# Performance work log

Measured on AMD Instinct MI355X. Metric: run time of the kernel, lower is better.

Reference implementation:

```python
import jax, jax.numpy as jnp
import numpy as np

B, O, T = 32, 256, 1024
D_OBJ = 512      # obj_input_dim
D_PRED = 512     # predicate_input_dim
HID = 512        # hidden_dim
P_OUT = 512      # predicate_output_dim
OBJ_OUT = 512    # object_output_dim
N_PRED_TYPES = 50
ORIGINAL_EDGE = 0
TRANSITIVE_EDGE = 1


def setup_inputs() -> dict:
    key = jax.random.key(0)
    ks = jax.random.split(key, 16)

    def kaiming(k, fan_in, fan_out):
        return jax.random.normal(k, (fan_in, fan_out), jnp.float32) * np.sqrt(2.0 / fan_in)

    n1_in = 2 * D_OBJ + D_PRED            # 1536
    n1_out = 2 * HID + P_OUT              # 1536
    return {
        "obj_vecs": jax.random.normal(ks[0], (B, O, D_OBJ), jnp.float32),
        "pred_vecs": jax.random.normal(ks[1], (B, T, D_PRED), jnp.float32),
        "W1a": kaiming(ks[2], n1_in, HID), "b1a": jnp.zeros((HID,), jnp.float32),
        "W1b": kaiming(ks[3], HID, n1_out), "b1b": jnp.zeros((n1_out,), jnp.float32),
        "W2a": kaiming(ks[4], HID, HID), "b2a": jnp.zeros((HID,), jnp.float32),
        "W2b": kaiming(ks[5], HID, OBJ_OUT), "b2b": jnp.zeros((OBJ_OUT,), jnp.float32),
        "pt_weights": jax.random.normal(ks[6], (N_PRED_TYPES,), jnp.float32),
        "edges": jax.random.randint(ks[7], (B, T, 2), 0, O, jnp.int32),
        "pred_indicators": jax.random.randint(ks[8], (B, T), 0, 2, jnp.int32).astype(bool),
        "triplet_type": jax.random.randint(ks[9], (B, T), 0, 2, jnp.int32),
        "predicate_ids": jax.random.randint(ks[10], (B, T), 0, N_PRED_TYPES, jnp.int32),
    }


def reference(obj_vecs, pred_vecs, W1a, b1a, W1b, b1b, W2a, b2a, W2b, b2b,
              pt_weights, edges, pred_indicators, triplet_type, predicate_ids):
    s_idx = edges[:, :, 0]  # [B,T]
    o_idx = edges[:, :, 1]

    # gather subject/object vectors: [B,T,D]
    cur_s = jnp.take_along_axis(obj_vecs, s_idx[:, :, None], axis=1)
    cur_o = jnp.take_along_axis(obj_vecs, o_idx[:, :, None], axis=1)
    cur_t = jnp.concatenate([cur_s, pred_vecs, cur_o], axis=-1)  # [B,T,2D+Dp]

    # net1: Linear-ReLU-Linear-ReLU
    h = jax.nn.relu(cur_t @ W1a + b1a)
    new_t = jax.nn.relu(h @ W1b + b1b)  # [B,T,2*HID+P_OUT]

    # confidence weighting
    pt_pred = jax.nn.sigmoid(pt_weights)  # [N_PRED_TYPES]
    conf = ((triplet_type == ORIGINAL_EDGE).astype(jnp.float32)
            + (triplet_type == TRANSITIVE_EDGE).astype(jnp.float32) * pt_pred[predicate_ids])  # [B,T]
    new_t = new_t * conf[:, :, None]

    new_s = new_t[:, :, :HID]
    new_p = new_t[:, :, HID:HID + P_OUT]
    new_o = new_t[:, :, HID + P_OUT:]

    mask = pred_indicators.astype(jnp.float32)  # [B,T]

    def pool_one(si, oi, sv, ov, cf, m):
        # masked scatter-add (equivalent to torch boolean-masked scatter_add)
        sums = (jax.ops.segment_sum(sv * m[:, None], si, num_segments=O)
                + jax.ops.segment_sum(ov * m[:, None], oi, num_segments=O))  # [O,HID]
        w = cf * m
        counts = (jax.ops.segment_sum(w, si, num_segments=O)
                  + jax.ops.segment_sum(w, oi, num_segments=O))  # [O]
        nz = counts > 0
        return jnp.where(nz[:, None], sums / jnp.where(nz, counts, 1.0)[:, None], sums)

    pooled = jax.vmap(pool_one)(s_idx, o_idx, new_s, new_o, conf, mask)  # [B,O,HID]

    # net2: Linear-ReLU-Linear-ReLU
    h2 = jax.nn.relu(pooled @ W2a + b2a)
    new_obj = jax.nn.relu(h2 @ W2b + b2b)  # [B,O,OBJ_OUT]

    return new_obj, new_p
```

## Files before the change

kernel.cpp:

```cpp
#include <hip/hip_runtime.h>
#include <hip/hip_bf16.h>
#include <cstdint>
#include <cstddef>

#define DEV __device__ __forceinline__

typedef __attribute__((ext_vector_type(8))) short  s8v;
typedef __attribute__((ext_vector_type(4))) float  f4v;
typedef __attribute__((ext_vector_type(4))) uint32_t u4v;

DEV unsigned short f2bf(float x) {
  union { float f; uint32_t u; } v; v.f = x;
  uint32_t u = v.u + 0x7FFFu + ((v.u >> 16) & 1u);
  return (unsigned short)(u >> 16);
}
DEV uint32_t cvtpk2(float lo, float hi) {
  uint32_t r;
  asm("v_cvt_pk_bf16_f32 %0, %1, %2" : "=v"(r) : "v"(lo), "v"(hi));
  return r;
}
DEV unsigned short f2bf_fast(float x) { return (unsigned short)cvtpk2(x, 0.f); }
DEV float bf2f(unsigned short b) {
  union { uint32_t u; float f; } v; v.u = ((uint32_t)b) << 16;
  return v.f;
}

DEV void async_copy16(void* lds, const void* g) {
  typedef __attribute__((address_space(3))) uint32_t lds_t;
  typedef const __attribute__((address_space(1))) uint32_t g_t;
  __builtin_amdgcn_global_load_lds((g_t*)g, (lds_t*)lds, 16, 0, 0);
}

#define WAITV4()    asm volatile("s_waitcnt vmcnt(4)" ::: "memory")
#define WAITV0()    asm volatile("s_waitcnt vmcnt(0)" ::: "memory")
#define MEMFENCE()  asm volatile("" ::: "memory")

constexpr int Bc = 32, Oc = 256, Tc = 1024;
constexpr int BM = 128, BN = 128, BK = 64;
constexpr int CSR_CAP = 46;

DEV void swz_mn(int nyb, int* mb, int* nb) {
  const int nwg = gridDim.x * gridDim.y;
  const int w   = blockIdx.x + blockIdx.y * gridDim.x;
  const int cpx = nwg >> 3;
  const int s   = (w & 7) * cpx + (w >> 3);
  *mb = s / nyb;
  *nb = s % nyb;
}

__global__ __launch_bounds__(256)
void cvt_k(const float* __restrict__ in, unsigned short* __restrict__ outp, int n8)
{
  const int i = blockIdx.x * 256 + threadIdx.x;
  if (i >= n8) return;
  const f4v v0 = *(const f4v*)(in + (size_t)i * 8);
  const f4v v1 = *(const f4v*)(in + (size_t)i * 8 + 4);
  u4v pk;
  pk.x = cvtpk2(v0.x, v0.y);
  pk.y = cvtpk2(v0.z, v0.w);
  pk.z = cvtpk2(v1.x, v1.y);
  pk.w = cvtpk2(v1.z, v1.w);
  *(u4v*)(outp + (size_t)i * 8) = pk;
}

#define READ_A(QM, DST) do {                                                    \
    _Pragma("unroll")                                                           \
    for (int i = 0; i < 4; ++i) {                                               \
      const int row = wm * 128 + ((QM) * 4 + i) * 16 + (lane & 15);             \
      _Pragma("unroll")                                                         \
      for (int kk = 0; kk < 2; ++kk) {                                          \
        const int c = kk * 4 + (lane >> 4);                                     \
        DST[i][kk] = *(const s8v*)(Ab_ + row * 128 + ((c ^ (row & 7)) << 4));   \
      }                                                                         \
    }                                                                           \
  } while (0)

#define READ_B(QN, DST) do {                                                    \
    _Pragma("unroll")                                                           \
    for (int j = 0; j < 2; ++j) {                                               \
      const int row = wn * 64 + ((QN) * 2 + j) * 16 + (lane & 15);              \
      _Pragma("unroll")                                                         \
      for (int kk = 0; kk < 2; ++kk) {                                          \
        const int c = kk * 4 + (lane >> 4);                                     \
        DST[j][kk] = *(const s8v*)(Bb_ + row * 128 + ((c ^ (row & 7)) << 4));   \
      }                                                                         \
    }                                                                           \
  } while (0)

#define SYNC_MFMA(QM, QN, AF, BF) do {                                          \
    MEMFENCE();                                                                 \
    __builtin_amdgcn_s_barrier();                                               \
    asm volatile("s_waitcnt lgkmcnt(0)" ::: "memory");                          \
    __builtin_amdgcn_sched_barrier(0);                                          \
    __builtin_amdgcn_s_setprio(1);                                              \
    _Pragma("unroll")                                                           \
    for (int i = 0; i < 4; ++i)                                                 \
      _Pragma("unroll")                                                         \
      for (int j = 0; j < 2; ++j)                                               \
        _Pragma("unroll")                                                       \
        for (int kk = 0; kk < 2; ++kk)                                          \
          acc[(QM) * 4 + i][(QN) * 2 + j] =                                     \
            __builtin_amdgcn_mfma_f32_16x16x32_bf16(                            \
              AF[i][kk], BF[j][kk], acc[(QM) * 4 + i][(QN) * 2 + j], 0, 0, 0);  \
    __builtin_amdgcn_s_setprio(0);                                              \
  } while (0)

#define ENDPHASE() do { MEMFENCE(); __builtin_amdgcn_s_barrier(); } while (0)

#define KTILE_BODY() do {                                                       \
    const int par = t & 1, px = par ^ 1;                                        \
    const char* Ab_ = smem + par * 65536;                                       \
    const char* Bb_ = Ab_ + 32768;                                              \
    const bool s1 = (t + 1 < nk), s2 = (t + 2 < nk);                            \
                                                                        \
    READ_A(0, af); READ_B(0, bf0);                                              \
    if (s1) stageA(px, 1, t + 1);                                               \
    SYNC_MFMA(0, 0, af, bf0);                                                   \
    ENDPHASE();                                                                 \
                                                                        \
    READ_B(1, bf1);                                                             \
    if (s1) stageB(px, 1, t + 1);                                               \
    SYNC_MFMA(0, 1, af, bf1);                                                   \
    ENDPHASE();                                                                 \
                                                                        \
    READ_A(1, af);                                                              \
    if (s2) stageA(par, 0, t + 2);                                              \
    SYNC_MFMA(1, 1, af, bf1);                                                   \
    ENDPHASE();                                                                 \
                                                                        \
    if (s2) stageB(par, 0, t + 2);                                              \
    SYNC_MFMA(1, 0, af, bf0);                                                   \
    if (s2) { WAITV4(); } else if (s1) { WAITV0(); }                            \
    ENDPHASE();                                                                 \
  } while (0)

template<int EPI>
__global__ __launch_bounds__(512, 2)
void gemm8_k(const unsigned short* __restrict__ Abf,
             const unsigned short* __restrict__ Bt,
             const float* __restrict__ bias,
             const float* __restrict__ conf,
             unsigned short* __restrict__ out_bf,
             float* __restrict__ out_f32,
             unsigned short* __restrict__ out_bf2,
             int M, int N, int K)
{
  __shared__ __align__(16) char smem[131072];

  const int tid = threadIdx.x, lane = tid & 63, wave = tid >> 6;
  const int wm = wave >> 2, wn = wave & 3;
  int mb, nb; swz_mn(gridDim.y, &mb, &nb);
  const int m0 = mb * 256, n0 = nb * 256;
  const int rl  = tid >> 3;
  const int cs8 = ((lane & 7) ^ (lane >> 3)) * 8;
  const int rB0 = (rl >> 5) * 64 + (rl & 31);

  const unsigned short* srcA = Abf + (size_t)(m0 + rl) * K + cs8;
  const unsigned short* srcB = Bt  + (size_t)(n0 + rB0) * K + cs8;

  auto stageA = [&](int p, int qm, int kt) {
    const int k0 = kt * 64;
    #pragma unroll
    for (int s = 0; s < 2; ++s)
      async_copy16(smem + p * 65536 + ((s * 128 + qm * 64 + wave * 8) << 7),
                   srcA + (size_t)(s * 128 + qm * 64) * K + k0);
  };
  auto stageB = [&](int p, int qn, int kt) {
    const int k0 = kt * 64;
    #pragma unroll
    for (int s = 0; s < 2; ++s)
      async_copy16(smem + p * 65536 + 32768 +
                     ((s * 128 + qn * 32 + (wave >> 2) * 64 + (wave & 3) * 8) << 7),
                   srcB + (size_t)(s * 128 + qn * 32) * K + k0);
  };

  f4v acc[8][4] = {};
  s8v af[4][2], bf0[2][2], bf1[2][2];
  const int nk = K / 64;

  stageA(0, 0, 0); stageB(0, 0, 0); stageA(0, 1, 0); stageB(0, 1, 0);
  stageA(1, 0, 1); stageB(1, 0, 1);
  WAITV4();
  MEMFENCE();
  __builtin_amdgcn_s_barrier();

  for (int t = 0; t < nk; ++t) KTILE_BODY();

  const int cn = lane & 15, rq4 = (lane >> 4) * 4;
  #pragma unroll
  for (int f = 0; f < 8; ++f) {
    const int gr0 = m0 + wm * 128 + f * 16 + rq4;
    #pragma unroll
    for (int g = 0; g < 4; ++g) {
      const int gc = n0 + wn * 64 + g * 16 + cn;
      const float bv = bias[gc];
      #pragma unroll
      for (int r = 0; r < 4; ++r) {
        float val = acc[f][g][r] + bv;
        val = val > 0.f ? val : 0.f;
        const int gr = gr0 + r;
        if (EPI == 1) {
          val *= conf[gr];
          if (gc < 512)        out_bf [(size_t)gr * 512 + gc]          = f2bf_fast(val);
          else if (gc < 1024)  out_f32[(size_t)gr * 512 + (gc - 512)]  = val;
          else                 out_bf2[(size_t)gr * 512 + (gc - 1024)] = f2bf_fast(val);
        } else {
          out_bf[(size_t)gr * N + gc] = f2bf_fast(val);
        }
      }
    }
  }
}

__global__ __launch_bounds__(512, 2)
void gemm8g_k(const unsigned short* __restrict__ objb,
              const unsigned short* __restrict__ predb,
              const int* __restrict__ edges,
              const unsigned short* __restrict__ Bt,
              const float* __restrict__ bias,
              unsigned short* __restrict__ outp)
{
  __shared__ __align__(16) char smem[131072];

  const int tid = threadIdx.x, lane = tid & 63, wave = tid >> 6;
  const int wm = wave >> 2, wn = wave & 3;
  int mb, nb; swz_mn(gridDim.y, &mb, &nb);
  const int m0 = mb * 256, n0 = nb * 256;
  const int rl  = tid >> 3;
  const int cs8 = ((lane & 7) ^ (lane >> 3)) * 8;
  const int rB0 = (rl >> 5) * 64 + (rl & 31);

  uint32_t offS[4], offP[4], offO[4];
  #pragma unroll
  for (int c2 = 0; c2 < 4; ++c2) {
    const int r = (c2 >> 1) * 128 + (c2 & 1) * 64 + rl;
    const int m = m0 + r;
    const int ob = (m >> 10) * Oc;
    offS[c2] = (uint32_t)((ob + edges[2 * m])     * 1024 + cs8 * 2);
    offO[c2] = (uint32_t)((ob + edges[2 * m + 1]) * 1024 + cs8 * 2);
    offP[c2] = (uint32_t)(m * 1024 + cs8 * 2);
  }
  const unsigned short* srcB = Bt + (size_t)(n0 + rB0) * 1536 + cs8;

  auto stageA = [&](int p, int qm, int kt) {
    const int reg = kt >> 3;
    const uint32_t koff = (uint32_t)(kt & 7) * 128u;
    #pragma unroll
    for (int s = 0; s < 2; ++s) {
      const int c2 = s * 2 + qm;
      const char* src;
      if (reg == 0)      src = (const char*)objb  + offS[c2] + koff;
      else if (reg == 1) src = (const char*)predb + offP[c2] + koff;
      else               src = (const char*)objb  + offO[c2] + koff;
      async_copy16(smem + p * 65536 + ((s * 128 + qm * 64 + wave * 8) << 7), src);
    }
  };
  auto stageB = [&](int p, int qn, int kt) {
    #pragma unroll
    for (int s = 0; s < 2; ++s)
      async_copy16(smem + p * 65536 + 32768 +
                     ((s * 128 + qn * 32 + (wave >> 2) * 64 + (wave & 3) * 8) << 7),
                   srcB + (size_t)(s * 128 + qn * 32) * 1536 + kt * 64);
  };

  f4v acc[8][4] = {};
  s8v af[4][2], bf0[2][2], bf1[2][2];
  constexpr int nk = 24;

  stageA(0, 0, 0); stageB(0, 0, 0); stageA(0, 1, 0); stageB(0, 1, 0);
  stageA(1, 0, 1); stageB(1, 0, 1);
  WAITV4();
  MEMFENCE();
  __builtin_amdgcn_s_barrier();

  for (int t = 0; t < nk; ++t) KTILE_BODY();

  const int cn = lane & 15, rq4 = (lane >> 4) * 4;
  #pragma unroll
  for (int f = 0; f < 8; ++f) {
    const int gr0 = m0 + wm * 128 + f * 16 + rq4;
    #pragma unroll
    for (int g = 0; g < 4; ++g) {
      const int gc = n0 + wn * 64 + g * 16 + cn;
      const float bv = bias[gc];
      #pragma unroll
      for (int r = 0; r < 4; ++r) {
        float val = acc[f][g][r] + bv;
        val = val > 0.f ? val : 0.f;
        outp[(size_t)(gr0 + r) * 512 + gc] = f2bf_fast(val);
      }
    }
  }
}

template<int EPI>
__global__ __launch_bounds__(256)
void gemm_k(const unsigned short* __restrict__ Abf,
            const unsigned short* __restrict__ Bt,
            const float* __restrict__ bias,
            unsigned short* __restrict__ out_bf,
            float* __restrict__ out_f32,
            int M, int N, int K)
{
  __shared__ __align__(16) char smem[BM * BK * 2 + BN * BK * 2];
  char* As = smem;
  char* Bs = smem + BM * BK * 2;

  const int tid  = threadIdx.x;
  const int lane = tid & 63;
  const int wave = tid >> 6;
  const int wm = wave >> 1, wn = wave & 1;
  int mb, nb; swz_mn(gridDim.y, &mb, &nb);
  const int m0 = mb * BM;
  const int n0 = nb * BN;

  f4v acc[4][4] = {};

  for (int k0 = 0; k0 < K; k0 += BK) {
    {
      const int r8 = lane >> 3;
      const int cs = (lane & 7) ^ r8;
      const unsigned short* src = Bt + (size_t)(n0 + wave * 32 + r8) * K + k0 + cs * 8;
      #pragma unroll
      for (int i = 0; i < 4; ++i)
        async_copy16(Bs + (wave * 32 + i * 8) * 128, src + (size_t)i * 8 * K);
      const unsigned short* srca = Abf + (size_t)(m0 + wave * 32 + r8) * K + k0 + cs * 8;
      #pragma unroll
      for (int i = 0; i < 4; ++i)
        async_copy16(As + (wave * 32 + i * 8) * 128, srca + (size_t)i * 8 * K);
    }
    __syncthreads();

    #pragma unroll
    for (int kk = 0; kk < 2; ++kk) {
      s8v af[4], bfv[4];
      #pragma unroll
      for (int i = 0; i < 4; ++i) {
        const int row = wm * 64 + i * 16 + (lane & 15);
        const int c = kk * 4 + (lane >> 4);
        af[i] = *(const s8v*)(As + row * 128 + ((c ^ (row & 7)) << 4));
      }
      #pragma unroll
      for (int j = 0; j < 4; ++j) {
        const int row = wn * 64 + j * 16 + (lane & 15);
        const int c = kk * 4 + (lane >> 4);
        bfv[j] = *(const s8v*)(Bs + row * 128 + ((c ^ (row & 7)) << 4));
      }
      #pragma unroll
      for (int i = 0; i < 4; ++i)
        #pragma unroll
        for (int j = 0; j < 4; ++j)
          acc[i][j] = __builtin_amdgcn_mfma_f32_16x16x32_bf16(af[i], bfv[j], acc[i][j], 0, 0, 0);
    }
    __syncthreads();
  }

  const int cn = lane & 15, rq4 = (lane >> 4) * 4;
  #pragma unroll
  for (int i = 0; i < 4; ++i) {
    const int gr0 = m0 + wm * 64 + i * 16 + rq4;
    #pragma unroll
    for (int j = 0; j < 4; ++j) {
      const int gc = n0 + wn * 64 + j * 16 + cn;
      const float bv = bias[gc];
      #pragma unroll
      for (int r = 0; r < 4; ++r) {
        float val = acc[i][j][r] + bv;
        val = val > 0.f ? val : 0.f;
        const int gr = gr0 + r;
        if (EPI == 0) out_bf[(size_t)gr * N + gc] = f2bf_fast(val);
        else          out_f32[(size_t)gr * N + gc] = val;
      }
    }
  }
}

__global__ void tcvt_k(const float* __restrict__ W, unsigned short* __restrict__ Wt,
                       int K, int N)
{
  __shared__ float tile[32][33];
  const int k0 = blockIdx.x * 32, n0 = blockIdx.y * 32;
  const int tx = threadIdx.x, ty = threadIdx.y;
  #pragma unroll
  for (int i = 0; i < 32; i += 8)
    tile[ty + i][tx] = W[(size_t)(k0 + ty + i) * N + (n0 + tx)];
  __syncthreads();
  #pragma unroll
  for (int i = 0; i < 32; i += 8)
    Wt[(size_t)(n0 + ty + i) * K + (k0 + tx)] = f2bf(tile[tx][ty + i]);
}

__global__ void detect_k(const unsigned char* __restrict__ mb, int* __restrict__ flag)
{
  __shared__ int any;
  if (threadIdx.x == 0) any = 0;
  __syncthreads();
  int local = 0;
  for (int i = threadIdx.x; i < Bc * Tc; i += 256)
    if ((i & 3) && mb[i]) local = 1;
  if (local) atomicOr(&any, 1);
  __syncthreads();
  if (threadIdx.x == 0) *flag = any;
}

__global__ void prep_k(const int* __restrict__ tt, const int* __restrict__ pid,
                       const float* __restrict__ ptw, const int* __restrict__ edges,
                       const void* __restrict__ mask, const int* __restrict__ u8flag,
                       float* __restrict__ conf, int* __restrict__ se, int* __restrict__ oe)
{
  const int m = blockIdx.x * 256 + threadIdx.x;
  const int t = tt[m];
  float c = 0.f;
  if (t == 0) c = 1.f;
  else if (t == 1) c = 1.f / (1.f + expf(-ptw[pid[m]]));
  conf[m] = c;
  bool mk;
  if (*u8flag) mk = ((const unsigned char*)mask)[m] != 0;
  else         mk = ((const int*)mask)[m] != 0;
  se[m] = mk ? edges[2 * m]     : -1;
  oe[m] = mk ? edges[2 * m + 1] : -1;
}

__global__ __launch_bounds__(256)
void csr2_k(const int* __restrict__ se, const int* __restrict__ oe,
            int* __restrict__ deg, int* __restrict__ slot)
{
  const int wid  = blockIdx.x * 4 + (threadIdx.x >> 6);
  const int b    = wid >> 8;
  const int u    = wid & 255;
  const int lane = threadIdx.x & 63;
  const int mb   = b * Tc;
  int* sl = slot + (size_t)wid * CSR_CAP;
  const unsigned long long lt = (1ull << lane) - 1ull;
  int cnt = 0;
  #pragma unroll 4
  for (int c = 0; c < 16; ++c) {
    const int t = c * 64 + lane;
    const int s = se[mb + t];
    const int o = oe[mb + t];
    const unsigned long long ms = __ballot(s == u);
    const unsigned long long mo = __ballot(o == u);
    if (s == u) {
      const int pos = cnt + (int)__popcll(ms & lt);
      if (pos < CSR_CAP) sl[pos] = 2 * t;
    }
    cnt += (int)__popcll(ms);
    if (o == u) {
      const int pos = cnt + (int)__popcll(mo & lt);
      if (pos < CSR_CAP) sl[pos] = 2 * t + 1;
    }
    cnt += (int)__popcll(mo);
  }
  if (lane == 0) deg[wid] = cnt < CSR_CAP ? cnt : CSR_CAP;
}

__global__ __launch_bounds__(256)
void pool2_k(const unsigned short* __restrict__ S, const unsigned short* __restrict__ Ov,
             const int* __restrict__ deg, const int* __restrict__ slot,
             const float* __restrict__ conf,
             unsigned short* __restrict__ pooled)
{
  const int bo = blockIdx.x;
  const int b  = bo >> 8;
  const int u  = threadIdx.x;
  const int d  = deg[bo];
  const int* sl = slot + (size_t)bo * CSR_CAP;
  float a0 = 0.f, a1 = 0.f, w = 0.f;
  for (int i = 0; i < d; ++i) {
    const int e = sl[i];
    const int t = e >> 1;
    const unsigned short* row = ((e & 1) ? Ov : S) + ((size_t)(b * Tc + t)) * 512;
    const uint32_t pr = *(const uint32_t*)(row + 2 * u);
    a0 += bf2f((unsigned short)pr);
    a1 += bf2f((unsigned short)(pr >> 16));
    w  += conf[b * Tc + t];
  }
  const float denom = (w > 0.f) ? w : 1.f;
  const size_t ob = (size_t)bo * 512;
  *(uint32_t*)(pooled + ob + 2 * u) = cvtpk2(a0 / denom, a1 / denom);
}

extern "C" void kernel_launch(void* const* d_in, const int* in_sizes, int n_in,
                              void* d_out, int out_size, void* d_ws, size_t ws_size,
                              hipStream_t stream)
{
  const float* obj  = (const float*)d_in[0];
  const float* pred = (const float*)d_in[1];
  const float* W1a  = (const float*)d_in[2];
  const float* b1a  = (const float*)d_in[3];
  const float* W1b  = (const float*)d_in[4];
  const float* b1b  = (const float*)d_in[5];
  const float* W2a  = (const float*)d_in[6];
  const float* b2a  = (const float*)d_in[7];
  const float* W2b  = (const float*)d_in[8];
  const float* b2b  = (const float*)d_in[9];
  const float* ptw  = (const float*)d_in[10];
  const int*   edges = (const int*)d_in[11];
  const void*  mask  = d_in[12];
  const int*   tt    = (const int*)d_in[13];
  const int*   pid   = (const int*)d_in[14];
  float* out = (float*)d_out;

  char* ws = (char*)d_ws;
  unsigned short* W1at = (unsigned short*)(ws + 0);
  unsigned short* W1bt = (unsigned short*)(ws + 1572864);
  unsigned short* W2at = (unsigned short*)(ws + 3145728);
  unsigned short* W2bt = (unsigned short*)(ws + 3670016);
  int* deg  = (int*)(ws + 0);
  int* slot = (int*)(ws + 32768);
  unsigned short* h    = (unsigned short*)(ws + 4194304);
  unsigned short* pooled = h;
  unsigned short* h2   = (unsigned short*)(ws + 12582912);
  unsigned short* news = (unsigned short*)(ws + 37748736);
  unsigned short* newo = (unsigned short*)(ws + 71303168);
  unsigned short* objb = news;
  unsigned short* predb = (unsigned short*)(ws + 46137344);
  float* conf = (float*)(ws + 104857600);
  int*   se   = (int*)(ws + 104988672);
  int*   oe   = (int*)(ws + 105119744);
  int* u8flag = (int*)(ws + 105250816);

  tcvt_k<<<dim3(48, 16), dim3(32, 8), 0, stream>>>(W1a, W1at, 1536, 512);
  tcvt_k<<<dim3(16, 48), dim3(32, 8), 0, stream>>>(W1b, W1bt, 512, 1536);
  tcvt_k<<<dim3(16, 16), dim3(32, 8), 0, stream>>>(W2a, W2at, 512, 512);
  tcvt_k<<<dim3(16, 16), dim3(32, 8), 0, stream>>>(W2b, W2bt, 512, 512);

  cvt_k<<<2048, 256, 0, stream>>>(obj,  objb,  Bc * Oc * 512 / 8);
  cvt_k<<<8192, 256, 0, stream>>>(pred, predb, Bc * Tc * 512 / 8);

  detect_k<<<1, 256, 0, stream>>>((const unsigned char*)mask, u8flag);
  prep_k<<<128, 256, 0, stream>>>(tt, pid, ptw, edges, mask, u8flag, conf, se, oe);

  gemm8g_k<<<dim3(128, 2), 512, 0, stream>>>(objb, predb, edges, W1at, b1a, h);

  csr2_k<<<2048, 256, 0, stream>>>(se, oe, deg, slot);

  gemm8_k<1><<<dim3(128, 6), 512, 0, stream>>>(
      h, W1bt, b1b, conf, news, out + 4194304, newo, 32768, 1536, 512);

  pool2_k<<<Bc * Oc, 256, 0, stream>>>(news, newo, deg, slot, conf, pooled);

  gemm_k<0><<<dim3(64, 4), 256, 0, stream>>>(
      pooled, W2at, b2a, h2, nullptr, 8192, 512, 512);

  gemm_k<2><<<dim3(64, 4), 256, 0, stream>>>(
      h2, W2bt, b2b, nullptr, out, 8192, 512, 512);
}
```

Before: 262.7 us.

## Replace 256x256 pipelined GEMM for net1 second layer with simpler 128x128 kernel

The second net1 GEMM (32768x1536x512) moves from the 256x256-tile, 8-wave, double-buffered async-copy kernel to a simpler 128x128-tile, 4-wave kernel with a single LDS buffer and two barriers per k-step. The grid grows from 768 to 3072 blocks, aiming at better wave balance across CUs and lower LDS and register pressure. The cost is less data reuse per tile and no overlap between global loads and MFMA work.

```diff
diff --git a/kernel.cpp b/kernel.cpp
--- a/kernel.cpp
+++ b/kernel.cpp
@@ -134,84 +134,6 @@
     ENDPHASE();                                                                 \
   } while (0)
 
-template<int EPI>
-__global__ __launch_bounds__(512, 2)
-void gemm8_k(const unsigned short* __restrict__ Abf,
-             const unsigned short* __restrict__ Bt,
-             const float* __restrict__ bias,
-             const float* __restrict__ conf,
-             unsigned short* __restrict__ out_bf,
-             float* __restrict__ out_f32,
-             unsigned short* __restrict__ out_bf2,
-             int M, int N, int K)
-{
-  __shared__ __align__(16) char smem[131072];
-
-  const int tid = threadIdx.x, lane = tid & 63, wave = tid >> 6;
-  const int wm = wave >> 2, wn = wave & 3;
-  int mb, nb; swz_mn(gridDim.y, &mb, &nb);
-  const int m0 = mb * 256, n0 = nb * 256;
-  const int rl  = tid >> 3;
-  const int cs8 = ((lane & 7) ^ (lane >> 3)) * 8;
-  const int rB0 = (rl >> 5) * 64 + (rl & 31);
-
-  const unsigned short* srcA = Abf + (size_t)(m0 + rl) * K + cs8;
-  const unsigned short* srcB = Bt  + (size_t)(n0 + rB0) * K + cs8;
-
-  auto stageA = [&](int p, int qm, int kt) {
-    const int k0 = kt * 64;
-    #pragma unroll
-    for (int s = 0; s < 2; ++s)
-      async_copy16(smem + p * 65536 + ((s * 128 + qm * 64 + wave * 8) << 7),
-                   srcA + (size_t)(s * 128 + qm * 64) * K + k0);
-  };
-  auto stageB = [&](int p, int qn, int kt) {
-    const int k0 = kt * 64;
-    #pragma unroll
-    for (int s = 0; s < 2; ++s)
-      async_copy16(smem + p * 65536 + 32768 +
-                     ((s * 128 + qn * 32 + (wave >> 2) * 64 + (wave & 3) * 8) << 7),
-                   srcB + (size_t)(s * 128 + qn * 32) * K + k0);
-  };
-
-  f4v acc[8][4] = {};
-  s8v af[4][2], bf0[2][2], bf1[2][2];
-  const int nk = K / 64;
-
-  stageA(0, 0, 0); stageB(0, 0, 0); stageA(0, 1, 0); stageB(0, 1, 0);
-  stageA(1, 0, 1); stageB(1, 0, 1);
-  WAITV4();
-  MEMFENCE();
-  __builtin_amdgcn_s_barrier();
-
-  for (int t = 0; t < nk; ++t) KTILE_BODY();
-
-  const int cn = lane & 15, rq4 = (lane >> 4) * 4;
-  #pragma unroll
-  for (int f = 0; f < 8; ++f) {
-    const int gr0 = m0 + wm * 128 + f * 16 + rq4;
-    #pragma unroll
-    for (int g = 0; g < 4; ++g) {
-      const int gc = n0 + wn * 64 + g * 16 + cn;
-      const float bv = bias[gc];
-      #pragma unroll
-      for (int r = 0; r < 4; ++r) {
-        float val = acc[f][g][r] + bv;
-        val = val > 0.f ? val : 0.f;
-        const int gr = gr0 + r;
-        if (EPI == 1) {
-          val *= conf[gr];
-          if (gc < 512)        out_bf [(size_t)gr * 512 + gc]          = f2bf_fast(val);
-          else if (gc < 1024)  out_f32[(size_t)gr * 512 + (gc - 512)]  = val;
-          else                 out_bf2[(size_t)gr * 512 + (gc - 1024)] = f2bf_fast(val);
-        } else {
-          out_bf[(size_t)gr * N + gc] = f2bf_fast(val);
-        }
-      }
-    }
-  }
-}
-
 __global__ __launch_bounds__(512, 2)
 void gemm8g_k(const unsigned short* __restrict__ objb,
               const unsigned short* __restrict__ predb,
@@ -288,6 +210,91 @@
         float val = acc[f][g][r] + bv;
         val = val > 0.f ? val : 0.f;
         outp[(size_t)(gr0 + r) * 512 + gc] = f2bf_fast(val);
+      }
+    }
+  }
+}
+
+__global__ __launch_bounds__(256)
+void gemm2_k(const unsigned short* __restrict__ Abf,
+             const unsigned short* __restrict__ Bt,
+             const float* __restrict__ bias,
+             const float* __restrict__ conf,
+             unsigned short* __restrict__ out_bf,
+             float* __restrict__ out_f32,
+             unsigned short* __restrict__ out_bf2,
+             int M, int N, int K)
+{
+  __shared__ __align__(16) char smem[BM * BK * 2 + BN * BK * 2];
+  char* As = smem;
+  char* Bs = smem + BM * BK * 2;
+
+  const int tid  = threadIdx.x;
+  const int lane = tid & 63;
+  const int wave = tid >> 6;
+  const int wm = wave >> 1, wn = wave & 1;
+  int mb, nb; swz_mn(gridDim.y, &mb, &nb);
+  const int m0 = mb * BM;
+  const int n0 = nb * BN;
+
+  f4v acc[4][4] = {};
+
+  for (int k0 = 0; k0 < K; k0 += BK) {
+    {
+      const int r8 = lane >> 3;
+      const int cs = (lane & 7) ^ r8;
+      const unsigned short* src = Bt + (size_t)(n0 + wave * 32 + r8) * K + k0 + cs * 8;
+      #pragma unroll
+      for (int i = 0; i < 4; ++i)
+        async_copy16(Bs + (wave * 32 + i * 8) * 128, src + (size_t)i * 8 * K);
+      const unsigned short* srca = Abf + (size_t)(m0 + wave * 32 + r8) * K + k0 + cs * 8;
+      #pragma unroll
+      for (int i = 0; i < 4; ++i)
+        async_copy16(As + (wave * 32 + i * 8) * 128, srca + (size_t)i * 8 * K);
+    }
+    __syncthreads();
+
+    #pragma unroll
+    for (int kk = 0; kk < 2; ++kk) {
+      s8v af[4], bfv[4];
+      #pragma unroll
+      for (int i = 0; i < 4; ++i) {
+        const int row = wm * 64 + i * 16 + (lane & 15);
+        const int c = kk * 4 + (lane >> 4);
+        af[i] = *(const s8v*)(As + row * 128 + ((c ^ (row & 7)) << 4));
+      }
+      #pragma unroll
+      for (int j = 0; j < 4; ++j) {
+        const int row = wn * 64 + j * 16 + (lane & 15);
+        const int c = kk * 4 + (lane >> 4);
+        bfv[j] = *(const s8v*)(Bs + row * 128 + ((c ^ (row & 7)) << 4));
+      }
+      #pragma unroll
+      for (int i = 0; i < 4; ++i)
+        #pragma unroll
+        for (int j = 0; j < 4; ++j)
+          acc[i][j] = __builtin_amdgcn_mfma_f32_16x16x32_bf16(af[i], bfv[j], acc[i][j], 0, 0, 0);
+    }
+    __syncthreads();
+  }
+
+  const int cn = lane & 15, rq4 = (lane >> 4) * 4;
+  #pragma unroll
+  for (int i = 0; i < 4; ++i) {
+    const int gr0 = m0 + wm * 64 + i * 16 + rq4;
+    #pragma unroll
+    for (int j = 0; j < 4; ++j) {
+      const int gc = n0 + wn * 64 + j * 16 + cn;
+      const float bv = bias[gc];
+      #pragma unroll
+      for (int r = 0; r < 4; ++r) {
+        float val = acc[i][j][r] + bv;
+        val = val > 0.f ? val : 0.f;
+        const int gr = gr0 + r;
+        val *= conf[gr];
+        if (gc < 512)        out_bf [(size_t)gr * 512 + gc]          = f2bf_fast(val);
+        else if (gc < 1024)  out_f32[(size_t)gr * 512 + (gc - 512)]  = val;
+        else                 out_bf2[(size_t)gr * 512 + (gc - 1024)] = f2bf_fast(val);
       }
     }
   }
@@ -535,7 +542,7 @@
 
   csr2_k<<<2048, 256, 0, stream>>>(se, oe, deg, slot);
 
-  gemm8_k<1><<<dim3(128, 6), 512, 0, stream>>>(
+  gemm2_k<<<dim3(256, 12), 256, 0, stream>>>(
       h, W1bt, b1b, conf, news, out + 4194304, newo, 32768, 1536, 512);
 
   pool2_k<<<Bc * Oc, 256, 0, stream>>>(news, newo, deg, slot, conf, pooled);
```

Result: faster. 256.9 us (-2.2%).
